# Kernel tuning notes

Hardware: AMD Instinct MI355X
Metric: run time of the kernel (lower is better)

The kernel has to match this reference:

```python
import jax, jax.numpy as jnp
import numpy as np

HEADS = 4

def setup_inputs() -> dict:
    B, L, D = 4, 2048, 256
    key = jax.random.key(0)
    k1, k2, k3, k4, k5, k6 = jax.random.split(key, 6)
    return {
        "atten": jax.random.normal(k1, (B, L, L), dtype=jnp.float32),
        "value": jax.random.normal(k2, (B, L, D), dtype=jnp.float32),
        "mask": jax.random.uniform(k3, (B, 1, L, L), dtype=jnp.float32),
        "padding_mask": jax.random.randint(k4, (B, L, L), 0, 2, dtype=jnp.int32),
        "Wv": jax.random.normal(k5, (D, D), dtype=jnp.float32) * 0.02,
        "bv": jnp.zeros((D,), dtype=jnp.float32),
        "Wo": jax.random.normal(k6, (D, D), dtype=jnp.float32) * 0.02,
        "bo": jnp.zeros((D,), dtype=jnp.float32),
    }

def reference(atten, value, mask, padding_mask, Wv, bv, Wo, bo):
    B, L, D = value.shape
    H = HEADS
    dk = D // H
    # to_value: Linear then split heads. N == 1 (value.unsqueeze(1) in torch).
    v = value @ Wv + bv                                   # (B, L, D)
    v = v.reshape(B, 1, L, H, dk).transpose(0, 3, 1, 2, 4)  # (B, H, N=1, L, dk)
    # externally supplied attention logits, two sequential masked fills
    a = atten[:, None, :, :]                              # (B, 1, L, L)
    a = jnp.where(mask < 0.5, jnp.finfo(a.dtype).min, a)
    a = jnp.where(padding_mask[:, None, :, :] == 0, -jnp.inf, a)
    a = jax.nn.softmax(a, axis=-1)                        # (B, 1, L, L)
    # dropout is identity in eval mode
    # einsum 'bhij,bhnjk->bhnik' with h=1 on a broadcast across H heads of v
    out = jnp.einsum('bij,bhnjk->bhnik', a[:, 0], v)      # (B, H, 1, L, dk)
    out = out.transpose(0, 2, 3, 1, 4).reshape(B, 1, L, D)
    out = out @ Wo + bo                                   # (B, 1, L, D)
    return out
```

## Files before the change

### kernel.cpp

```cpp
#include <hip/hip_runtime.h>
#include <hip/hip_bf16.h>
#include <math.h>

#define L 2048
#define D 256
#define NEG_FLT_MAX (-3.402823466e38f)

typedef __attribute__((ext_vector_type(8))) short bf16x8;
typedef __attribute__((ext_vector_type(4))) float f32x4;
typedef __attribute__((ext_vector_type(4))) int i32x4;

__device__ __forceinline__ unsigned short f2bf(float f) {
    union { float f; unsigned int u; } v; v.f = f;
    unsigned int r = v.u + 0x7FFFu + ((v.u >> 16) & 1u);
    return (unsigned short)(r >> 16);
}

__global__ __launch_bounds__(256, 4) void prep_kernel(
    const float* __restrict__ value, const float* __restrict__ Wv,
    const float* __restrict__ bv, const float* __restrict__ Wo,
    unsigned short* __restrict__ Vt, unsigned short* __restrict__ Wot) {
    const int tid = threadIdx.x;
    const int wave = tid >> 6, lane = tid & 63;
    const int lm = lane & 15, q = lane >> 4;
    const int rh = wave >> 1;
    const int nh = wave & 1;
    const int m0 = blockIdx.x * 32;
    const int n0 = blockIdx.y * 64;

    __shared__ __align__(16) unsigned short Wlds[64][264];

    {
        int bid = blockIdx.y * 256 + blockIdx.x;
        if (tid < 64) {
            int e = bid * 64 + tid;
            int k = e >> 8, n = e & 255;
            Wot[n * 256 + k] = f2bf(Wo[k * 256 + n]);
        }
    }
    {
        int krow = tid >> 4;
        int nrel = (tid & 15) * 4;
#pragma unroll
        for (int p = 0; p < 16; p++) {
            int k = p * 16 + krow;
            f32x4 w = *reinterpret_cast<const f32x4*>(Wv + (size_t)k * 256 + n0 + nrel);
            Wlds[nrel + 0][k] = f2bf(w[0]);
            Wlds[nrel + 1][k] = f2bf(w[1]);
            Wlds[nrel + 2][k] = f2bf(w[2]);
            Wlds[nrel + 3][k] = f2bf(w[3]);
        }
    }
    __syncthreads();

    const int nl0 = nh * 32 + lm;
    const int nl1 = nh * 32 + 16 + lm;
    const int arow = m0 + rh * 16 + lm;

    f32x4 acc[2];
    acc[0] = (f32x4)(0.f); acc[1] = (f32x4)(0.f);

    const float* ap = value + (size_t)arow * 256;
    f32x4 pa0 = *reinterpret_cast<const f32x4*>(ap + q * 8);
    f32x4 pa1 = *reinterpret_cast<const f32x4*>(ap + q * 8 + 4);

    for (int k0 = 0; k0 < 256; k0 += 32) {
        f32x4 a0 = pa0, a1 = pa1;
        if (k0 < 224) {
            int kq = k0 + 32 + q * 8;
            pa0 = *reinterpret_cast<const f32x4*>(ap + kq);
            pa1 = *reinterpret_cast<const f32x4*>(ap + kq + 4);
        }
        bf16x8 b0 = *reinterpret_cast<const bf16x8*>(&Wlds[nl0][k0 + q * 8]);
        bf16x8 b1 = *reinterpret_cast<const bf16x8*>(&Wlds[nl1][k0 + q * 8]);
        bf16x8 afr;
#pragma unroll
        for (int e = 0; e < 4; e++) afr[e] = (short)f2bf(a0[e]);
#pragma unroll
        for (int e = 0; e < 4; e++) afr[4 + e] = (short)f2bf(a1[e]);
        acc[0] = __builtin_amdgcn_mfma_f32_16x16x32_bf16(afr, b0, acc[0], 0, 0, 0);
        acc[1] = __builtin_amdgcn_mfma_f32_16x16x32_bf16(afr, b1, acc[1], 0, 0, 0);
    }

    int mrow = m0 + rh * 16 + q * 4;
    int b = mrow >> 11;
    int j = mrow & 2047;
#pragma unroll
    for (int nf = 0; nf < 2; nf++) {
        int n = n0 + nh * 32 + nf * 16 + lm;
        float bias_n = bv[n];
        const f32x4& a = acc[nf];
        unsigned short* dst = Vt + (size_t)b * (D * L) + (size_t)n * L + j;
        ushort4 pk;
        pk.x = f2bf(a[0] + bias_n);
        pk.y = f2bf(a[1] + bias_n);
        pk.z = f2bf(a[2] + bias_n);
        pk.w = f2bf(a[3] + bias_n);
        *reinterpret_cast<ushort4*>(dst) = pk;
    }
}

__global__ __launch_bounds__(256, 4) void attn_kernel(
    const float* __restrict__ atten, const float* __restrict__ mask,
    const int* __restrict__ pad, const unsigned short* __restrict__ Vt,
    float* __restrict__ part) {
    const int bid = blockIdx.x;
    const int g = (bid & 7) * 128 + (bid >> 3);
    const int b = g >> 8;
    const int js = (g >> 7) & 1;
    const int i0 = (g & 127) * 16;
    const int tid = threadIdx.x;
    const int wave = tid >> 6, lane = tid & 63;
    const int lm = lane & 15, q = lane >> 4;
    const int r = tid >> 4;
    const int c4 = (tid & 15) * 4;

    __shared__ __align__(16) unsigned short Plds[2][16][72];

    f32x4 acc[4];
#pragma unroll
    for (int nf = 0; nf < 4; nf++) acc[nf] = (f32x4)(0.f);
    float lsum = 0.f;

    const size_t rowoff = ((size_t)(b * L + i0 + r)) * L + js * 1024 + c4;
    const float* at_p = atten + rowoff;
    const float* mk_p = mask + rowoff;
    const int*   pd_p = pad + rowoff;
    const unsigned short* vt_b = Vt + (size_t)b * (D * L) + js * 1024;

    f32x4 pa = *reinterpret_cast<const f32x4*>(at_p);
    f32x4 pm = *reinterpret_cast<const f32x4*>(mk_p);
    i32x4 pp = *reinterpret_cast<const i32x4*>(pd_p);

    for (int jt = 0; jt < 16; jt++) {
        const int j0 = jt * 64;
        bf16x8 bfr[2][4];
#pragma unroll
        for (int kk = 0; kk < 2; kk++)
#pragma unroll
            for (int nf = 0; nf < 4; nf++) {
                int n = wave * 64 + nf * 16 + lm;
                bfr[kk][nf] = *reinterpret_cast<const bf16x8*>(
                    vt_b + (size_t)n * L + j0 + kk * 32 + q * 8);
            }
        f32x4 a = pa, k = pm;
        i32x4 p = pp;
        if (jt < 15) {
            pa = *reinterpret_cast<const f32x4*>(at_p + j0 + 64);
            pm = *reinterpret_cast<const f32x4*>(mk_p + j0 + 64);
            pp = *reinterpret_cast<const i32x4*>(pd_p + j0 + 64);
        }
        ushort4 pk;
        float p0, p1, p2, p3;
        {
            float s0 = (k[0] < 0.5f) ? NEG_FLT_MAX : a[0];
            s0 = (p[0] == 0) ? -INFINITY : s0; p0 = __expf(s0);
            float s1 = (k[1] < 0.5f) ? NEG_FLT_MAX : a[1];
            s1 = (p[1] == 0) ? -INFINITY : s1; p1 = __expf(s1);
            float s2 = (k[2] < 0.5f) ? NEG_FLT_MAX : a[2];
            s2 = (p[2] == 0) ? -INFINITY : s2; p2 = __expf(s2);
            float s3 = (k[3] < 0.5f) ? NEG_FLT_MAX : a[3];
            s3 = (p[3] == 0) ? -INFINITY : s3; p3 = __expf(s3);
        }
        lsum += (p0 + p1) + (p2 + p3);
        pk.x = f2bf(p0); pk.y = f2bf(p1); pk.z = f2bf(p2); pk.w = f2bf(p3);

        const int par = jt & 1;
        *reinterpret_cast<ushort4*>(&Plds[par][r][c4]) = pk;
        __syncthreads();

#pragma unroll
        for (int kk = 0; kk < 2; kk++) {
            bf16x8 afr = *reinterpret_cast<const bf16x8*>(
                &Plds[par][lm][kk * 32 + q * 8]);
#pragma unroll
            for (int nf = 0; nf < 4; nf++)
                acc[nf] = __builtin_amdgcn_mfma_f32_16x16x32_bf16(
                    afr, bfr[kk][nf], acc[nf], 0, 0, 0);
        }
    }

    lsum += __shfl_xor(lsum, 1);
    lsum += __shfl_xor(lsum, 2);
    lsum += __shfl_xor(lsum, 4);
    lsum += __shfl_xor(lsum, 8);

    float* pbase = part + (size_t)g * 4112;
#pragma unroll
    for (int nf = 0; nf < 4; nf++) {
        int n = wave * 64 + nf * 16 + lm;
#pragma unroll
        for (int rg = 0; rg < 4; rg++)
            pbase[(q * 4 + rg) * 256 + n] = acc[nf][rg];
    }
    if ((tid & 15) == 0) pbase[4096 + r] = lsum;
}

__global__ __launch_bounds__(256, 2) void gemm_out_kernel(
    const float* __restrict__ part,
    const unsigned short* __restrict__ Wt,
    const float* __restrict__ bias,
    float* __restrict__ Cout) {
    const int wave = threadIdx.x >> 6;
    const int lane = threadIdx.x & 63;
    const int lm = lane & 15, q = lane >> 4;
    const int m0 = blockIdx.x * 64;
    const int n0 = blockIdx.y * 64;
    const int arow = m0 + wave * 16 + lm;
    const int b = arow >> 11;
    const int rg16 = (arow & 2047) >> 4;
    const int r_in = arow & 15;
    const float* pb0 = part + (size_t)(b * 256 + rg16) * 4112;
    const float* pb1 = pb0 + (size_t)128 * 4112;

    float linv = 1.f / (pb0[4096 + r_in] + pb1[4096 + r_in]);

    int ncol[4];
#pragma unroll
    for (int nf = 0; nf < 4; nf++) ncol[nf] = n0 + nf * 16 + lm;

    f32x4 acc[4];
#pragma unroll
    for (int nf = 0; nf < 4; nf++) acc[nf] = (f32x4)(0.f);

    for (int k0 = 0; k0 < 256; k0 += 32) {
        int kq = k0 + q * 8;
        bf16x8 bfr[4];
#pragma unroll
        for (int nf = 0; nf < 4; nf++)
            bfr[nf] = *reinterpret_cast<const bf16x8*>(Wt + (size_t)ncol[nf] * 256 + kq);
        f32x4 s0 = *reinterpret_cast<const f32x4*>(pb0 + r_in * 256 + kq)
                 + *reinterpret_cast<const f32x4*>(pb1 + r_in * 256 + kq);
        f32x4 s1 = *reinterpret_cast<const f32x4*>(pb0 + r_in * 256 + kq + 4)
                 + *reinterpret_cast<const f32x4*>(pb1 + r_in * 256 + kq + 4);
        bf16x8 afr;
#pragma unroll
        for (int e = 0; e < 4; e++) afr[e] = (short)f2bf(s0[e] * linv);
#pragma unroll
        for (int e = 0; e < 4; e++) afr[4 + e] = (short)f2bf(s1[e] * linv);
#pragma unroll
        for (int nf = 0; nf < 4; nf++)
            acc[nf] = __builtin_amdgcn_mfma_f32_16x16x32_bf16(
                afr, bfr[nf], acc[nf], 0, 0, 0);
    }

    int mrow = m0 + wave * 16 + q * 4;
#pragma unroll
    for (int nf = 0; nf < 4; nf++) {
        int n = ncol[nf];
        float bias_n = bias[n];
#pragma unroll
        for (int rg = 0; rg < 4; rg++)
            Cout[(size_t)(mrow + rg) * 256 + n] = acc[nf][rg] + bias_n;
    }
}

extern "C" void kernel_launch(void* const* d_in, const int* in_sizes, int n_in,
                              void* d_out, int out_size, void* d_ws, size_t ws_size,
                              hipStream_t stream) {
    (void)in_sizes; (void)n_in; (void)out_size; (void)ws_size;
    const float* atten = (const float*)d_in[0];
    const float* value = (const float*)d_in[1];
    const float* mask  = (const float*)d_in[2];
    const int*   pad   = (const int*)d_in[3];
    const float* Wv    = (const float*)d_in[4];
    const float* bv    = (const float*)d_in[5];
    const float* Wo    = (const float*)d_in[6];
    const float* bo    = (const float*)d_in[7];
    float* out = (float*)d_out;

    char* ws = (char*)d_ws;
    unsigned short* Vt  = (unsigned short*)(ws);
    unsigned short* Wot = (unsigned short*)(ws + 4194304);
    float* part = (float*)(ws + 4325376);

    prep_kernel<<<dim3(256, 4), 256, 0, stream>>>(value, Wv, bv, Wo, Vt, Wot);
    attn_kernel<<<1024, 256, 0, stream>>>(atten, mask, pad, Vt, part);
    gemm_out_kernel<<<dim3(128, 4), 256, 0, stream>>>(part, Wot, bo, out);
}
```

Baseline: 274.7 us.

## Split attn kernel into full-row softmax staging phase then barrier-free MFMA loop

```diff
diff --git a/kernel.cpp b/kernel.cpp
--- a/kernel.cpp
+++ b/kernel.cpp
@@ -4,7 +4,6 @@
 
 #define L 2048
 #define D 256
-#define NEG_FLT_MAX (-3.402823466e38f)
 
 typedef __attribute__((ext_vector_type(8))) short bf16x8;
 typedef __attribute__((ext_vector_type(4))) float f32x4;
@@ -112,80 +111,65 @@
     const int tid = threadIdx.x;
     const int wave = tid >> 6, lane = tid & 63;
     const int lm = lane & 15, q = lane >> 4;
-    const int r = tid >> 4;
-    const int c4 = (tid & 15) * 4;
-
-    __shared__ __align__(16) unsigned short Plds[2][16][72];
+
+    __shared__ __align__(16) unsigned short Plds[16][1032];
+
+    float* pbase = part + (size_t)g * 4112;
+
+    {
+        const int r = tid >> 4;
+        const int c4 = (tid & 15) * 4;
+        const size_t rowbase = ((size_t)(b * L + i0 + r)) * L + js * 1024 + c4;
+        const float* at_r = atten + rowbase;
+        const float* mk_r = mask + rowbase;
+        const int*   pd_r = pad + rowbase;
+        float lsum = 0.f;
+#pragma unroll 2
+        for (int jt = 0; jt < 16; jt++) {
+            const int jb = jt * 64;
+            f32x4 av = *reinterpret_cast<const f32x4*>(at_r + jb);
+            f32x4 mv = *reinterpret_cast<const f32x4*>(mk_r + jb);
+            i32x4 pv = *reinterpret_cast<const i32x4*>(pd_r + jb);
+            float pe[4];
+#pragma unroll
+            for (int e = 0; e < 4; e++) {
+                float p = __expf(av[e]);
+                p = (mv[e] < 0.5f) ? 0.f : p;
+                p = (pv[e] == 0) ? 0.f : p;
+                pe[e] = p;
+            }
+            lsum += (pe[0] + pe[1]) + (pe[2] + pe[3]);
+            ushort4 pk;
+            pk.x = f2bf(pe[0]); pk.y = f2bf(pe[1]);
+            pk.z = f2bf(pe[2]); pk.w = f2bf(pe[3]);
+            *reinterpret_cast<ushort4*>(&Plds[r][jb + c4]) = pk;
+        }
+        lsum += __shfl_xor(lsum, 1);
+        lsum += __shfl_xor(lsum, 2);
+        lsum += __shfl_xor(lsum, 4);
+        lsum += __shfl_xor(lsum, 8);
+        if ((tid & 15) == 0) pbase[4096 + r] = lsum;
+    }
+    __syncthreads();
 
     f32x4 acc[4];
 #pragma unroll
     for (int nf = 0; nf < 4; nf++) acc[nf] = (f32x4)(0.f);
-    float lsum = 0.f;
-
-    const size_t rowoff = ((size_t)(b * L + i0 + r)) * L + js * 1024 + c4;
-    const float* at_p = atten + rowoff;
-    const float* mk_p = mask + rowoff;
-    const int*   pd_p = pad + rowoff;
-    const unsigned short* vt_b = Vt + (size_t)b * (D * L) + js * 1024;
-
-    f32x4 pa = *reinterpret_cast<const f32x4*>(at_p);
-    f32x4 pm = *reinterpret_cast<const f32x4*>(mk_p);
-    i32x4 pp = *reinterpret_cast<const i32x4*>(pd_p);
-
-    for (int jt = 0; jt < 16; jt++) {
-        const int j0 = jt * 64;
-        bf16x8 bfr[2][4];
-#pragma unroll
-        for (int kk = 0; kk < 2; kk++)
-#pragma unroll
-            for (int nf = 0; nf < 4; nf++) {
-                int n = wave * 64 + nf * 16 + lm;
-                bfr[kk][nf] = *reinterpret_cast<const bf16x8*>(
-                    vt_b + (size_t)n * L + j0 + kk * 32 + q * 8);
-            }
-        f32x4 a = pa, k = pm;
-        i32x4 p = pp;
-        if (jt < 15) {
-            pa = *reinterpret_cast<const f32x4*>(at_p + j0 + 64);
-            pm = *reinterpret_cast<const f32x4*>(mk_p + j0 + 64);
-            pp = *reinterpret_cast<const i32x4*>(pd_p + j0 + 64);
-        }
-        ushort4 pk;
-        float p0, p1, p2, p3;
-        {
-            float s0 = (k[0] < 0.5f) ? NEG_FLT_MAX : a[0];
-            s0 = (p[0] == 0) ? -INFINITY : s0; p0 = __expf(s0);
-            float s1 = (k[1] < 0.5f) ? NEG_FLT_MAX : a[1];
-            s1 = (p[1] == 0) ? -INFINITY : s1; p1 = __expf(s1);
-            float s2 = (k[2] < 0.5f) ? NEG_FLT_MAX : a[2];
-            s2 = (p[2] == 0) ? -INFINITY : s2; p2 = __expf(s2);
-            float s3 = (k[3] < 0.5f) ? NEG_FLT_MAX : a[3];
-            s3 = (p[3] == 0) ? -INFINITY : s3; p3 = __expf(s3);
-        }
-        lsum += (p0 + p1) + (p2 + p3);
-        pk.x = f2bf(p0); pk.y = f2bf(p1); pk.z = f2bf(p2); pk.w = f2bf(p3);
-
-        const int par = jt & 1;
-        *reinterpret_cast<ushort4*>(&Plds[par][r][c4]) = pk;
-        __syncthreads();
-
-#pragma unroll
-        for (int kk = 0; kk < 2; kk++) {
-            bf16x8 afr = *reinterpret_cast<const bf16x8*>(
-                &Plds[par][lm][kk * 32 + q * 8]);
-#pragma unroll
-            for (int nf = 0; nf < 4; nf++)
-                acc[nf] = __builtin_amdgcn_mfma_f32_16x16x32_bf16(
-                    afr, bfr[kk][nf], acc[nf], 0, 0, 0);
-        }
-    }
-
-    lsum += __shfl_xor(lsum, 1);
-    lsum += __shfl_xor(lsum, 2);
-    lsum += __shfl_xor(lsum, 4);
-    lsum += __shfl_xor(lsum, 8);
-
-    float* pbase = part + (size_t)g * 4112;
+
+    const unsigned short* vt_b = Vt + (size_t)b * (D * L) + js * 1024 + q * 8;
+    const unsigned short* prow = &Plds[lm][q * 8];
+#pragma unroll 2
+    for (int j0 = 0; j0 < 1024; j0 += 32) {
+        bf16x8 afr = *reinterpret_cast<const bf16x8*>(prow + j0);
+#pragma unroll
+        for (int nf = 0; nf < 4; nf++) {
+            int n = wave * 64 + nf * 16 + lm;
+            bf16x8 bfr = *reinterpret_cast<const bf16x8*>(vt_b + (size_t)n * L + j0);
+            acc[nf] = __builtin_amdgcn_mfma_f32_16x16x32_bf16(
+                afr, bfr, acc[nf], 0, 0, 0);
+        }
+    }
+
 #pragma unroll
     for (int nf = 0; nf < 4; nf++) {
         int n = wave * 64 + nf * 16 + lm;
@@ -193,7 +177,6 @@
         for (int rg = 0; rg < 4; rg++)
             pbase[(q * 4 + rg) * 256 + n] = acc[nf][rg];
     }
-    if ((tid & 15) == 0) pbase[4096 + r] = lsum;
 }
 
 __global__ __launch_bounds__(256, 2) void gemm_out_kernel(
```

Result: slower. 290.5 us (+5.7%).
